# Kernel optimization log

Hardware: AMD Instinct MI355X
Metric: run time of the kernel (lower is better)

Reference implementation:

```python
import jax, jax.numpy as jnp
import numpy as np

N_NODES = 50000
N_EDGES = 800000
IN_CH = 1024
OUT_CH = 256


def setup_inputs() -> dict:
    key = jax.random.key(0)
    ks = jax.random.split(key, 7)
    x = jax.random.normal(ks[0], (N_NODES, IN_CH), dtype=jnp.float32)
    src_index = jax.random.randint(ks[1], (N_EDGES,), 0, N_NODES, dtype=jnp.int32)
    tar_index = jax.random.randint(ks[2], (N_EDGES,), 0, N_NODES, dtype=jnp.int32)
    edge_weight = jax.random.uniform(ks[3], (N_EDGES,), dtype=jnp.float32)
    self_edge_weight = jax.random.uniform(ks[4], (N_NODES,), dtype=jnp.float32)
    # Linear layer params (torch.nn.Linear: y = x @ W.T + b)
    bound = 1.0 / np.sqrt(IN_CH)
    W = jax.random.uniform(ks[5], (OUT_CH, IN_CH), dtype=jnp.float32, minval=-bound, maxval=bound)
    b = jax.random.uniform(ks[6], (OUT_CH,), dtype=jnp.float32, minval=-bound, maxval=bound)
    return {"x": x, "W": W, "b": b, "src_index": src_index, "tar_index": tar_index,
            "edge_weight": edge_weight, "self_edge_weight": self_edge_weight}


def reference(x, W, b, src_index, tar_index, edge_weight, self_edge_weight):
    # dense linear projection: [N, in] -> [N, out]
    h = jnp.einsum('ni,oi->no', x, W) + b
    # edge aggregation: out[t] += w_e * h[src_e]  (SpMM-like gather/scatter)
    msgs = h[src_index] * edge_weight[:, None]          # [E, out]
    agg = jax.ops.segment_sum(msgs, tar_index, num_segments=h.shape[0])
    # self-loop term
    return agg + self_edge_weight[:, None] * h
```

## Files before the change

### kernel.cpp

```cpp
#include <hip/hip_runtime.h>
#include <hip/hip_bf16.h>

#define N_NODES 50000
#define N_EDGES 800000
#define IN_CH 1024
#define OUT_CH 256
#define NBLK 196

typedef __attribute__((ext_vector_type(8))) short bf16x8;
typedef __attribute__((ext_vector_type(4))) float f32x4;

__device__ inline unsigned short f2bf(float f) {
  union { float f; unsigned int u; } v; v.f = f;
  unsigned int r = v.u + 0x7fffu + ((v.u >> 16) & 1u);
  return (unsigned short)(r >> 16);
}
__device__ inline float bf2f(unsigned short u) {
  union { unsigned int u; float f; } v; v.u = ((unsigned int)u) << 16;
  return v.f;
}

__global__ __launch_bounds__(256) void prep_hist(const float* __restrict__ W,
                                                 unsigned short* __restrict__ Wb,
                                                 const int* __restrict__ tar,
                                                 int* __restrict__ counts) {
  const int b = blockIdx.x, t = threadIdx.x;
  if (b < 256) {
    const int i4 = (b * 256 + t) * 4;
    float4 f = *(const float4*)(W + i4);
    *(ushort4*)(Wb + i4) = make_ushort4(f2bf(f.x), f2bf(f.y), f2bf(f.z), f2bf(f.w));
  } else {
    const int e = (b - 256) * 256 + t;
    if (e < N_EDGES) atomicAdd(&counts[tar[e]], 1);
  }
}

__global__ __launch_bounds__(256, 4) void gemm_proj(
    const float* __restrict__ X, const unsigned short* __restrict__ Wb,
    const float* __restrict__ bias, unsigned short* __restrict__ Hb)
{
  __shared__ unsigned short lds_a[2][64][32];
  __shared__ unsigned short lds_b[2][128][32];

  const int tid  = threadIdx.x;
  const int lane = tid & 63;
  const int w    = tid >> 6;
  const int wr   = w >> 1, wc = w & 1;
  const int gm0  = blockIdx.x * 64;
  const int gn0  = blockIdx.y * 128;

  const int ar = tid >> 3;
  const int ac = (tid & 7) * 4;
  const int br = tid >> 2;
  const int bc = (tid & 3) * 8;

  const int arow0 = gm0 + ar, arow1 = gm0 + ar + 32;
  const bool aok0 = arow0 < N_NODES, aok1 = arow1 < N_NODES;
  const float* xp0 = X + (size_t)arow0 * IN_CH + ac;
  const float* xp1 = X + (size_t)arow1 * IN_CH + ac;
  const unsigned short* wp0 = Wb + (size_t)(gn0 + br) * IN_CH + bc;
  const unsigned short* wp1 = Wb + (size_t)(gn0 + br + 64) * IN_CH + bc;

  f32x4 acc[2][4];
  #pragma unroll
  for (int i = 0; i < 2; i++)
    #pragma unroll
    for (int j = 0; j < 4; j++) acc[i][j] = (f32x4)0.0f;

  float4 avA0, avA1, avB0, avB1;
  bf16x8 bvA0, bvA1, bvB0, bvB1;

#define LOADR(KS, AV0, AV1, BV0, BV1)                                          \
  {                                                                            \
    const int k0_ = (KS) * 32;                                                 \
    AV0 = aok0 ? *(const float4*)(xp0 + k0_) : make_float4(0.f, 0.f, 0.f, 0.f);\
    AV1 = aok1 ? *(const float4*)(xp1 + k0_) : make_float4(0.f, 0.f, 0.f, 0.f);\
    BV0 = *(const bf16x8*)(wp0 + k0_);                                         \
    BV1 = *(const bf16x8*)(wp1 + k0_);                                         \
  }

#define WRITER(BUF, AV0, AV1, BV0, BV1)                                        \
  {                                                                            \
    *(ushort4*)&lds_a[BUF][ar][ac] =                                           \
        make_ushort4(f2bf(AV0.x), f2bf(AV0.y), f2bf(AV0.z), f2bf(AV0.w));      \
    *(ushort4*)&lds_a[BUF][ar + 32][ac] =                                      \
        make_ushort4(f2bf(AV1.x), f2bf(AV1.y), f2bf(AV1.z), f2bf(AV1.w));      \
    *(bf16x8*)&lds_b[BUF][br][bc]      = BV0;                                  \
    *(bf16x8*)&lds_b[BUF][br + 64][bc] = BV1;                                  \
  }

#define COMPUTE(BUF)                                                           \
  {                                                                            \
    const int l15_ = lane & 15;                                                \
    const int kb_  = (lane >> 4) * 8;                                          \
    bf16x8 a0 = *(const bf16x8*)&lds_a[BUF][wr * 32 + l15_][kb_];              \
    bf16x8 a1 = *(const bf16x8*)&lds_a[BUF][wr * 32 + 16 + l15_][kb_];         \
    bf16x8 b0 = *(const bf16x8*)&lds_b[BUF][wc * 64 + l15_][kb_];              \
    bf16x8 b1 = *(const bf16x8*)&lds_b[BUF][wc * 64 + 16 + l15_][kb_];         \
    bf16x8 b2 = *(const bf16x8*)&lds_b[BUF][wc * 64 + 32 + l15_][kb_];         \
    bf16x8 b3 = *(const bf16x8*)&lds_b[BUF][wc * 64 + 48 + l15_][kb_];         \
    acc[0][0] = __builtin_amdgcn_mfma_f32_16x16x32_bf16(a0, b0, acc[0][0], 0, 0, 0); \
    acc[0][1] = __builtin_amdgcn_mfma_f32_16x16x32_bf16(a0, b1, acc[0][1], 0, 0, 0); \
    acc[0][2] = __builtin_amdgcn_mfma_f32_16x16x32_bf16(a0, b2, acc[0][2], 0, 0, 0); \
    acc[0][3] = __builtin_amdgcn_mfma_f32_16x16x32_bf16(a0, b3, acc[0][3], 0, 0, 0); \
    acc[1][0] = __builtin_amdgcn_mfma_f32_16x16x32_bf16(a1, b0, acc[1][0], 0, 0, 0); \
    acc[1][1] = __builtin_amdgcn_mfma_f32_16x16x32_bf16(a1, b1, acc[1][1], 0, 0, 0); \
    acc[1][2] = __builtin_amdgcn_mfma_f32_16x16x32_bf16(a1, b2, acc[1][2], 0, 0, 0); \
    acc[1][3] = __builtin_amdgcn_mfma_f32_16x16x32_bf16(a1, b3, acc[1][3], 0, 0, 0); \
  }

  LOADR(0, avA0, avA1, bvA0, bvA1);
  WRITER(0, avA0, avA1, bvA0, bvA1);
  LOADR(1, avB0, avB1, bvB0, bvB1);
  __syncthreads();

  for (int ks = 0; ks < 32; ks += 2) {
    if (ks + 2 < 32) LOADR(ks + 2, avA0, avA1, bvA0, bvA1);
    COMPUTE(0);
    WRITER(1, avB0, avB1, bvB0, bvB1);
    __syncthreads();
    if (ks + 3 < 32) LOADR(ks + 3, avB0, avB1, bvB0, bvB1);
    COMPUTE(1);
    if (ks + 2 < 32) WRITER(0, avA0, avA1, bvA0, bvA1);
    __syncthreads();
  }
#undef LOADR
#undef WRITER
#undef COMPUTE

  float bj[4];
  #pragma unroll
  for (int j = 0; j < 4; j++)
    bj[j] = bias[gn0 + wc * 64 + j * 16 + (lane & 15)];

  #pragma unroll
  for (int i = 0; i < 2; i++) {
    const int grow_base = gm0 + wr * 32 + i * 16 + ((lane >> 4) << 2);
    #pragma unroll
    for (int r = 0; r < 4; r++) {
      const int grow = grow_base + r;
      if (grow < N_NODES) {
        #pragma unroll
        for (int j = 0; j < 4; j++) {
          const int gcol = gn0 + wc * 64 + j * 16 + (lane & 15);
          Hb[(size_t)grow * OUT_CH + gcol] = f2bf(acc[i][j][r] + bj[j]);
        }
      }
    }
  }
}

__global__ __launch_bounds__(256) void scan_block(const int* __restrict__ counts,
                                                  int* __restrict__ offsets,
                                                  int* __restrict__ blocksum) {
  __shared__ int wsum[4];
  const int tid = threadIdx.x, lane = tid & 63, wv = tid >> 6;
  const int i = blockIdx.x * 256 + tid;
  const int v = (i < N_NODES) ? counts[i] : 0;
  int s = v;
  #pragma unroll
  for (int off = 1; off < 64; off <<= 1) {
    int t = __shfl_up(s, off, 64);
    if (lane >= off) s += t;
  }
  if (lane == 63) wsum[wv] = s;
  __syncthreads();
  if (tid == 0) {
    int c = 0;
    #pragma unroll
    for (int k = 0; k < 4; k++) { int t = wsum[k]; wsum[k] = c; c += t; }
  }
  __syncthreads();
  const int excl = wsum[wv] + s - v;
  if (i < N_NODES) offsets[i] = excl;
  if (tid == 255) blocksum[blockIdx.x] = excl + v;
}

__global__ __launch_bounds__(256) void scan_sums(int* __restrict__ blocksum,
                                                 int* __restrict__ offsets) {
  __shared__ int wsum[4];
  const int tid = threadIdx.x, lane = tid & 63, wv = tid >> 6;
  const int v = (tid < NBLK) ? blocksum[tid] : 0;
  int s = v;
  #pragma unroll
  for (int off = 1; off < 64; off <<= 1) {
    int t = __shfl_up(s, off, 64);
    if (lane >= off) s += t;
  }
  if (lane == 63) wsum[wv] = s;
  __syncthreads();
  if (tid == 0) {
    int c = 0;
    #pragma unroll
    for (int k = 0; k < 4; k++) { int t = wsum[k]; wsum[k] = c; c += t; }
  }
  __syncthreads();
  const int excl = wsum[wv] + s - v;
  if (tid < NBLK) blocksum[tid] = excl;
  if (tid == 255) offsets[N_NODES] = excl;
}

__global__ __launch_bounds__(256) void finalize_offsets(int* __restrict__ offsets,
                                                        const int* __restrict__ blocksum,
                                                        int* __restrict__ cursor) {
  const int i = blockIdx.x * 256 + threadIdx.x;
  if (i < N_NODES) {
    const int off = offsets[i] + blocksum[i >> 8];
    offsets[i] = off;
    cursor[i] = off;
  }
}

__global__ __launch_bounds__(256) void fill_csr(const int* __restrict__ src,
                                                const int* __restrict__ tar,
                                                const float* __restrict__ ew,
                                                int* __restrict__ cursor,
                                                int2* __restrict__ edata) {
  int e = blockIdx.x * blockDim.x + threadIdx.x;
  if (e >= N_EDGES) return;
  const int t = tar[e];
  const int p = atomicAdd(&cursor[t], 1);
  edata[p] = make_int2(src[e], __float_as_int(ew[e]));
}

__global__ __launch_bounds__(256) void node_agg(
    const unsigned short* __restrict__ Hb, const int* __restrict__ offsets,
    const int2* __restrict__ edata, const float* __restrict__ sw,
    float* __restrict__ OUT)
{
  const int wid = (blockIdx.x * blockDim.x + threadIdx.x) >> 6;
  if (wid >= N_NODES) return;
  const int lane = threadIdx.x & 63;
  const int e0 = offsets[wid];
  const int e1 = offsets[wid + 1];

  float a0 = 0.f, a1 = 0.f, a2 = 0.f, a3 = 0.f;

  for (int base = e0; base < e1; base += 64) {
    const int avail = e1 - base;
    int2 d = make_int2(0, 0);
    if (lane < avail) d = edata[base + lane];
    const int n = (avail < 64) ? avail : 64;
    int j = 0;
    for (; j + 4 <= n; j += 4) {
      const int   s0 = __shfl(d.x, j, 64),     s1 = __shfl(d.x, j + 1, 64);
      const int   s2 = __shfl(d.x, j + 2, 64), s3 = __shfl(d.x, j + 3, 64);
      const float w0 = __int_as_float(__shfl(d.y, j, 64));
      const float w1 = __int_as_float(__shfl(d.y, j + 1, 64));
      const float w2 = __int_as_float(__shfl(d.y, j + 2, 64));
      const float w3 = __int_as_float(__shfl(d.y, j + 3, 64));
      const ushort4 h0 = *(const ushort4*)(Hb + (size_t)s0 * OUT_CH + lane * 4);
      const ushort4 h1 = *(const ushort4*)(Hb + (size_t)s1 * OUT_CH + lane * 4);
      const ushort4 h2 = *(const ushort4*)(Hb + (size_t)s2 * OUT_CH + lane * 4);
      const ushort4 h3 = *(const ushort4*)(Hb + (size_t)s3 * OUT_CH + lane * 4);
      a0 += w0 * bf2f(h0.x) + w1 * bf2f(h1.x) + w2 * bf2f(h2.x) + w3 * bf2f(h3.x);
      a1 += w0 * bf2f(h0.y) + w1 * bf2f(h1.y) + w2 * bf2f(h2.y) + w3 * bf2f(h3.y);
      a2 += w0 * bf2f(h0.z) + w1 * bf2f(h1.z) + w2 * bf2f(h2.z) + w3 * bf2f(h3.z);
      a3 += w0 * bf2f(h0.w) + w1 * bf2f(h1.w) + w2 * bf2f(h2.w) + w3 * bf2f(h3.w);
    }
    for (; j < n; j++) {
      const int   s = __shfl(d.x, j, 64);
      const float wgt = __int_as_float(__shfl(d.y, j, 64));
      const ushort4 h = *(const ushort4*)(Hb + (size_t)s * OUT_CH + lane * 4);
      a0 += wgt * bf2f(h.x); a1 += wgt * bf2f(h.y);
      a2 += wgt * bf2f(h.z); a3 += wgt * bf2f(h.w);
    }
  }

  const float swv = sw[wid];
  const ushort4 hs = *(const ushort4*)(Hb + (size_t)wid * OUT_CH + lane * 4);
  float4 o;
  o.x = a0 + swv * bf2f(hs.x);
  o.y = a1 + swv * bf2f(hs.y);
  o.z = a2 + swv * bf2f(hs.z);
  o.w = a3 + swv * bf2f(hs.w);
  *(float4*)(OUT + (size_t)wid * OUT_CH + lane * 4) = o;
}

extern "C" void kernel_launch(void* const* d_in, const int* in_sizes, int n_in,
                              void* d_out, int out_size, void* d_ws, size_t ws_size,
                              hipStream_t stream) {
  const float* x   = (const float*)d_in[0];
  const float* W   = (const float*)d_in[1];
  const float* b   = (const float*)d_in[2];
  const int*   src = (const int*)d_in[3];
  const int*   tar = (const int*)d_in[4];
  const float* ew  = (const float*)d_in[5];
  const float* sw  = (const float*)d_in[6];
  float* out = (float*)d_out;

  char* ws = (char*)d_ws;
  size_t o = 0;
  unsigned short* Wb = (unsigned short*)(ws + o);
  o += (size_t)OUT_CH * IN_CH * 2;          o = (o + 255) & ~(size_t)255;
  unsigned short* Hb = (unsigned short*)(ws + o);
  o += (size_t)N_NODES * OUT_CH * 2;        o = (o + 255) & ~(size_t)255;
  int* counts   = (int*)(ws + o); o += (size_t)N_NODES * 4;       o = (o + 255) & ~(size_t)255;
  int* offsets  = (int*)(ws + o); o += (size_t)(N_NODES + 1) * 4; o = (o + 255) & ~(size_t)255;
  int* cursor   = (int*)(ws + o); o += (size_t)N_NODES * 4;       o = (o + 255) & ~(size_t)255;
  int* blocksum = (int*)(ws + o); o += (size_t)NBLK * 4;          o = (o + 255) & ~(size_t)255;
  int2* edata   = (int2*)(ws + o);

  hipMemsetAsync(counts, 0, (size_t)N_NODES * 4, stream);
  prep_hist<<<256 + (N_EDGES + 255) / 256, 256, 0, stream>>>(W, Wb, tar, counts);
  scan_block<<<NBLK, 256, 0, stream>>>(counts, offsets, blocksum);
  scan_sums<<<1, 256, 0, stream>>>(blocksum, offsets);
  finalize_offsets<<<NBLK, 256, 0, stream>>>(offsets, blocksum, cursor);
  fill_csr<<<(N_EDGES + 255) / 256, 256, 0, stream>>>(src, tar, ew, cursor, edata);

  dim3 g1((N_NODES + 63) / 64, OUT_CH / 128);
  gemm_proj<<<g1, 256, 0, stream>>>(x, Wb, b, Hb);

  const long long nthreads = (long long)N_NODES * 64;
  node_agg<<<(int)((nthreads + 255) / 256), 256, 0, stream>>>(Hb, offsets, edata, sw, out);
}
```

Before: 244.0 us.

## Deepen X prefetch pipeline to three stages and use packed bf16 conversion

The GEMM projection now prefetches X tiles three k-steps ahead in a 3-slot register ring, while W stays two steps ahead. The loop is fully unrolled with one barrier per step. The f32-to-bf16 conversion of X uses the hardware v_cvt_pk_bf16_f32 instruction instead of the manual rounding sequence. More registers are needed, so launch bounds drop from 4 to 3 blocks per CU, trading occupancy for deeper latency hiding of the X loads.

```diff
diff --git a/kernel.cpp b/kernel.cpp
--- a/kernel.cpp
+++ b/kernel.cpp
@@ -18,6 +18,11 @@
 __device__ inline float bf2f(unsigned short u) {
   union { unsigned int u; float f; } v; v.u = ((unsigned int)u) << 16;
   return v.f;
+}
+__device__ inline unsigned int cvtpk_bf16(float a, float b) {
+  unsigned int r;
+  asm("v_cvt_pk_bf16_f32 %0, %1, %2" : "=v"(r) : "v"(a), "v"(b));
+  return r;
 }
 
 __global__ __launch_bounds__(256) void prep_hist(const float* __restrict__ W,
@@ -35,7 +40,7 @@
   }
 }
 
-__global__ __launch_bounds__(256, 4) void gemm_proj(
+__global__ __launch_bounds__(256, 3) void gemm_proj(
     const float* __restrict__ X, const unsigned short* __restrict__ Wb,
     const float* __restrict__ bias, unsigned short* __restrict__ Hb)
 {
@@ -67,28 +72,34 @@
     #pragma unroll
     for (int j = 0; j < 4; j++) acc[i][j] = (f32x4)0.0f;
 
-  float4 avA0, avA1, avB0, avB1;
-  bf16x8 bvA0, bvA1, bvB0, bvB1;
-
-#define LOADR(KS, AV0, AV1, BV0, BV1)                                          \
+  float4 pa[3][2];
+  bf16x8 pb[2][2];
+
+#define LOADA(KS, SL)                                                          \
   {                                                                            \
     const int k0_ = (KS) * 32;                                                 \
-    AV0 = aok0 ? *(const float4*)(xp0 + k0_) : make_float4(0.f, 0.f, 0.f, 0.f);\
-    AV1 = aok1 ? *(const float4*)(xp1 + k0_) : make_float4(0.f, 0.f, 0.f, 0.f);\
-    BV0 = *(const bf16x8*)(wp0 + k0_);                                         \
-    BV1 = *(const bf16x8*)(wp1 + k0_);                                         \
-  }
-
-#define WRITER(BUF, AV0, AV1, BV0, BV1)                                        \
+    pa[SL][0] = aok0 ? *(const float4*)(xp0 + k0_)                             \
+                     : make_float4(0.f, 0.f, 0.f, 0.f);                        \
+    pa[SL][1] = aok1 ? *(const float4*)(xp1 + k0_)                             \
+                     : make_float4(0.f, 0.f, 0.f, 0.f);                        \
+  }
+#define LOADB(KS, SL)                                                          \
   {                                                                            \
-    *(ushort4*)&lds_a[BUF][ar][ac] =                                           \
-        make_ushort4(f2bf(AV0.x), f2bf(AV0.y), f2bf(AV0.z), f2bf(AV0.w));      \
-    *(ushort4*)&lds_a[BUF][ar + 32][ac] =                                      \
-        make_ushort4(f2bf(AV1.x), f2bf(AV1.y), f2bf(AV1.z), f2bf(AV1.w));      \
-    *(bf16x8*)&lds_b[BUF][br][bc]      = BV0;                                  \
-    *(bf16x8*)&lds_b[BUF][br + 64][bc] = BV1;                                  \
-  }
-
+    const int k0_ = (KS) * 32;                                                 \
+    pb[SL][0] = *(const bf16x8*)(wp0 + k0_);                                   \
+    pb[SL][1] = *(const bf16x8*)(wp1 + k0_);                                   \
+  }
+#define WRITER(BUF, SA, SB)                                                    \
+  {                                                                            \
+    *(uint2*)&lds_a[BUF][ar][ac] =                                             \
+        make_uint2(cvtpk_bf16(pa[SA][0].x, pa[SA][0].y),                       \
+                   cvtpk_bf16(pa[SA][0].z, pa[SA][0].w));                      \
+    *(uint2*)&lds_a[BUF][ar + 32][ac] =                                        \
+        make_uint2(cvtpk_bf16(pa[SA][1].x, pa[SA][1].y),                       \
+                   cvtpk_bf16(pa[SA][1].z, pa[SA][1].w));                      \
+    *(bf16x8*)&lds_b[BUF][br][bc]      = pb[SB][0];                            \
+    *(bf16x8*)&lds_b[BUF][br + 64][bc] = pb[SB][1];                            \
+  }
 #define COMPUTE(BUF)                                                           \
   {                                                                            \
     const int l15_ = lane & 15;                                                \
@@ -109,22 +120,21 @@
     acc[1][3] = __builtin_amdgcn_mfma_f32_16x16x32_bf16(a1, b3, acc[1][3], 0, 0, 0); \
   }
 
-  LOADR(0, avA0, avA1, bvA0, bvA1);
-  WRITER(0, avA0, avA1, bvA0, bvA1);
-  LOADR(1, avB0, avB1, bvB0, bvB1);
-  __syncthreads();
-
-  for (int ks = 0; ks < 32; ks += 2) {
-    if (ks + 2 < 32) LOADR(ks + 2, avA0, avA1, bvA0, bvA1);
-    COMPUTE(0);
-    WRITER(1, avB0, avB1, bvB0, bvB1);
+  LOADA(0, 0); LOADA(1, 1); LOADA(2, 2);
+  LOADB(0, 0); LOADB(1, 1);
+  WRITER(0, 0, 0);
+  __syncthreads();
+
+  #pragma unroll
+  for (int ks = 0; ks < 32; ks++) {
+    if (ks + 3 < 32) LOADA(ks + 3, (ks + 3) % 3);
+    if (ks + 2 < 32) LOADB(ks + 2, ks & 1);
+    COMPUTE(ks & 1);
+    if (ks + 1 < 32) WRITER((ks + 1) & 1, (ks + 1) % 3, (ks + 1) & 1);
     __syncthreads();
-    if (ks + 3 < 32) LOADR(ks + 3, avB0, avB1, bvB0, bvB1);
-    COMPUTE(1);
-    if (ks + 2 < 32) WRITER(0, avA0, avA1, bvA0, bvA1);
-    __syncthreads();
-  }
-#undef LOADR
+  }
+#undef LOADA
+#undef LOADB
 #undef WRITER
 #undef COMPUTE
 
```

Measured after the change: 236.3 us. 3.2% less time.

## Deepen GEMM K-tile to 64 with swizzled LDS and unroll gather by 8

Applied to the files above, without the earlier changes.

The projection GEMM now stages 64-wide K slices per step instead of 32, halving the number of barrier-separated iterations. Its LDS layout gains an XOR swizzle to avoid bank conflicts, and the float-to-bf16 conversion uses the packed v_cvt_pk_bf16_f32 instruction. The edge-gather loop now issues eight row loads before accumulating, up from four, to increase memory-level parallelism. The costs are more LDS and registers per block, which the launch bound lowers from 4 to 3 blocks per CU, reducing occupancy.

```diff
diff --git a/kernel.cpp b/kernel.cpp
--- a/kernel.cpp
+++ b/kernel.cpp
@@ -18,6 +18,11 @@
 __device__ inline float bf2f(unsigned short u) {
   union { unsigned int u; float f; } v; v.u = ((unsigned int)u) << 16;
   return v.f;
+}
+__device__ inline unsigned int cvtpk_bf16(float a, float b) {
+  unsigned int r;
+  asm("v_cvt_pk_bf16_f32 %0, %1, %2" : "=v"(r) : "v"(a), "v"(b));
+  return r;
 }
 
 __global__ __launch_bounds__(256) void prep_hist(const float* __restrict__ W,
@@ -35,12 +40,12 @@
   }
 }
 
-__global__ __launch_bounds__(256, 4) void gemm_proj(
+__global__ __launch_bounds__(256, 3) void gemm_proj(
     const float* __restrict__ X, const unsigned short* __restrict__ Wb,
     const float* __restrict__ bias, unsigned short* __restrict__ Hb)
 {
-  __shared__ unsigned short lds_a[2][64][32];
-  __shared__ unsigned short lds_b[2][128][32];
+  __shared__ unsigned short lds_a[2][64][64];
+  __shared__ unsigned short lds_b[2][128][64];
 
   const int tid  = threadIdx.x;
   const int lane = tid & 63;
@@ -48,18 +53,19 @@
   const int wr   = w >> 1, wc = w & 1;
   const int gm0  = blockIdx.x * 64;
   const int gn0  = blockIdx.y * 128;
-
-  const int ar = tid >> 3;
-  const int ac = (tid & 7) * 4;
-  const int br = tid >> 2;
-  const int bc = (tid & 3) * 8;
-
-  const int arow0 = gm0 + ar, arow1 = gm0 + ar + 32;
-  const bool aok0 = arow0 < N_NODES, aok1 = arow1 < N_NODES;
-  const float* xp0 = X + (size_t)arow0 * IN_CH + ac;
-  const float* xp1 = X + (size_t)arow1 * IN_CH + ac;
-  const unsigned short* wp0 = Wb + (size_t)(gn0 + br) * IN_CH + bc;
-  const unsigned short* wp1 = Wb + (size_t)(gn0 + br + 64) * IN_CH + bc;
+  const int l15  = lane & 15;
+  const int hi   = lane >> 4;
+
+  const int ar  = tid >> 2;
+  const int ac0 = (tid & 3) * 2;
+  const int br  = tid >> 1;
+  const int bc0 = (tid & 1) * 4;
+
+  const int  arow = gm0 + ar;
+  const bool aok  = arow < N_NODES;
+  const float* xp = X + (size_t)arow * IN_CH;
+  const unsigned short* wp = Wb + (size_t)(gn0 + br) * IN_CH;
+  const float4 fz = make_float4(0.f, 0.f, 0.f, 0.f);
 
   f32x4 acc[2][4];
   #pragma unroll
@@ -67,61 +73,81 @@
     #pragma unroll
     for (int j = 0; j < 4; j++) acc[i][j] = (f32x4)0.0f;
 
-  float4 avA0, avA1, avB0, avB1;
-  bf16x8 bvA0, bvA1, bvB0, bvB1;
-
-#define LOADR(KS, AV0, AV1, BV0, BV1)                                          \
+  float4 pa[2][4];
+  bf16x8 pbv[2][4];
+
+#define LOADR(KS, S)                                                           \
   {                                                                            \
-    const int k0_ = (KS) * 32;                                                 \
-    AV0 = aok0 ? *(const float4*)(xp0 + k0_) : make_float4(0.f, 0.f, 0.f, 0.f);\
-    AV1 = aok1 ? *(const float4*)(xp1 + k0_) : make_float4(0.f, 0.f, 0.f, 0.f);\
-    BV0 = *(const bf16x8*)(wp0 + k0_);                                         \
-    BV1 = *(const bf16x8*)(wp1 + k0_);                                         \
-  }
-
-#define WRITER(BUF, AV0, AV1, BV0, BV1)                                        \
+    const int k0_ = (KS) * 64;                                                 \
+    const float* xa_ = xp + k0_ + ac0 * 8;                                     \
+    pa[S][0] = aok ? *(const float4*)(xa_)      : fz;                          \
+    pa[S][1] = aok ? *(const float4*)(xa_ + 4)  : fz;                          \
+    pa[S][2] = aok ? *(const float4*)(xa_ + 8)  : fz;                          \
+    pa[S][3] = aok ? *(const float4*)(xa_ + 12) : fz;                          \
+    const unsigned short* wb_ = wp + k0_ + bc0 * 8;                            \
+    pbv[S][0] = *(const bf16x8*)(wb_);                                         \
+    pbv[S][1] = *(const bf16x8*)(wb_ + 8);                                     \
+    pbv[S][2] = *(const bf16x8*)(wb_ + 16);                                    \
+    pbv[S][3] = *(const bf16x8*)(wb_ + 24);                                    \
+  }
+
+#define WRITER(BUF, S)                                                         \
   {                                                                            \
-    *(ushort4*)&lds_a[BUF][ar][ac] =                                           \
-        make_ushort4(f2bf(AV0.x), f2bf(AV0.y), f2bf(AV0.z), f2bf(AV0.w));      \
-    *(ushort4*)&lds_a[BUF][ar + 32][ac] =                                      \
-        make_ushort4(f2bf(AV1.x), f2bf(AV1.y), f2bf(AV1.z), f2bf(AV1.w));      \
-    *(bf16x8*)&lds_b[BUF][br][bc]      = BV0;                                  \
-    *(bf16x8*)&lds_b[BUF][br + 64][bc] = BV1;                                  \
+    const int pc0_ = ac0 ^ (ar & 7);                                           \
+    const int pc1_ = (ac0 + 1) ^ (ar & 7);                                     \
+    union { unsigned int u[4]; bf16x8 v; } ta_;                                \
+    ta_.u[0] = cvtpk_bf16(pa[S][0].x, pa[S][0].y);                             \
+    ta_.u[1] = cvtpk_bf16(pa[S][0].z, pa[S][0].w);                             \
+    ta_.u[2] = cvtpk_bf16(pa[S][1].x, pa[S][1].y);                             \
+    ta_.u[3] = cvtpk_bf16(pa[S][1].z, pa[S][1].w);                             \
+    *(bf16x8*)&lds_a[BUF][ar][pc0_ * 8] = ta_.v;                               \
+    ta_.u[0] = cvtpk_bf16(pa[S][2].x, pa[S][2].y);                             \
+    ta_.u[1] = cvtpk_bf16(pa[S][2].z, pa[S][2].w);                             \
+    ta_.u[2] = cvtpk_bf16(pa[S][3].x, pa[S][3].y);                             \
+    ta_.u[3] = cvtpk_bf16(pa[S][3].z, pa[S][3].w);                             \
+    *(bf16x8*)&lds_a[BUF][ar][pc1_ * 8] = ta_.v;                               \
+    _Pragma("unroll")                                                          \
+    for (int q = 0; q < 4; q++) {                                              \
+      const int pcb_ = (bc0 + q) ^ (br & 7);                                   \
+      *(bf16x8*)&lds_b[BUF][br][pcb_ * 8] = pbv[S][q];                         \
+    }                                                                          \
   }
 
 #define COMPUTE(BUF)                                                           \
   {                                                                            \
-    const int l15_ = lane & 15;                                                \
-    const int kb_  = (lane >> 4) * 8;                                          \
-    bf16x8 a0 = *(const bf16x8*)&lds_a[BUF][wr * 32 + l15_][kb_];              \
-    bf16x8 a1 = *(const bf16x8*)&lds_a[BUF][wr * 32 + 16 + l15_][kb_];         \
-    bf16x8 b0 = *(const bf16x8*)&lds_b[BUF][wc * 64 + l15_][kb_];              \
-    bf16x8 b1 = *(const bf16x8*)&lds_b[BUF][wc * 64 + 16 + l15_][kb_];         \
-    bf16x8 b2 = *(const bf16x8*)&lds_b[BUF][wc * 64 + 32 + l15_][kb_];         \
-    bf16x8 b3 = *(const bf16x8*)&lds_b[BUF][wc * 64 + 48 + l15_][kb_];         \
-    acc[0][0] = __builtin_amdgcn_mfma_f32_16x16x32_bf16(a0, b0, acc[0][0], 0, 0, 0); \
-    acc[0][1] = __builtin_amdgcn_mfma_f32_16x16x32_bf16(a0, b1, acc[0][1], 0, 0, 0); \
-    acc[0][2] = __builtin_amdgcn_mfma_f32_16x16x32_bf16(a0, b2, acc[0][2], 0, 0, 0); \
-    acc[0][3] = __builtin_amdgcn_mfma_f32_16x16x32_bf16(a0, b3, acc[0][3], 0, 0, 0); \
-    acc[1][0] = __builtin_amdgcn_mfma_f32_16x16x32_bf16(a1, b0, acc[1][0], 0, 0, 0); \
-    acc[1][1] = __builtin_amdgcn_mfma_f32_16x16x32_bf16(a1, b1, acc[1][1], 0, 0, 0); \
-    acc[1][2] = __builtin_amdgcn_mfma_f32_16x16x32_bf16(a1, b2, acc[1][2], 0, 0, 0); \
-    acc[1][3] = __builtin_amdgcn_mfma_f32_16x16x32_bf16(a1, b3, acc[1][3], 0, 0, 0); \
-  }
-
-  LOADR(0, avA0, avA1, bvA0, bvA1);
-  WRITER(0, avA0, avA1, bvA0, bvA1);
-  LOADR(1, avB0, avB1, bvB0, bvB1);
-  __syncthreads();
-
-  for (int ks = 0; ks < 32; ks += 2) {
-    if (ks + 2 < 32) LOADR(ks + 2, avA0, avA1, bvA0, bvA1);
+    _Pragma("unroll")                                                          \
+    for (int kk2 = 0; kk2 < 2; kk2++) {                                        \
+      const int pc_ = ((kk2 << 2) + hi) ^ (l15 & 7);                           \
+      bf16x8 a0 = *(const bf16x8*)&lds_a[BUF][wr * 32 + l15][pc_ * 8];         \
+      bf16x8 a1 = *(const bf16x8*)&lds_a[BUF][wr * 32 + 16 + l15][pc_ * 8];    \
+      bf16x8 b0 = *(const bf16x8*)&lds_b[BUF][wc * 64 + l15][pc_ * 8];         \
+      bf16x8 b1 = *(const bf16x8*)&lds_b[BUF][wc * 64 + 16 + l15][pc_ * 8];    \
+      bf16x8 b2 = *(const bf16x8*)&lds_b[BUF][wc * 64 + 32 + l15][pc_ * 8];    \
+      bf16x8 b3 = *(const bf16x8*)&lds_b[BUF][wc * 64 + 48 + l15][pc_ * 8];    \
+      acc[0][0] = __builtin_amdgcn_mfma_f32_16x16x32_bf16(a0, b0, acc[0][0], 0, 0, 0); \
+      acc[0][1] = __builtin_amdgcn_mfma_f32_16x16x32_bf16(a0, b1, acc[0][1], 0, 0, 0); \
+      acc[0][2] = __builtin_amdgcn_mfma_f32_16x16x32_bf16(a0, b2, acc[0][2], 0, 0, 0); \
+      acc[0][3] = __builtin_amdgcn_mfma_f32_16x16x32_bf16(a0, b3, acc[0][3], 0, 0, 0); \
+      acc[1][0] = __builtin_amdgcn_mfma_f32_16x16x32_bf16(a1, b0, acc[1][0], 0, 0, 0); \
+      acc[1][1] = __builtin_amdgcn_mfma_f32_16x16x32_bf16(a1, b1, acc[1][1], 0, 0, 0); \
+      acc[1][2] = __builtin_amdgcn_mfma_f32_16x16x32_bf16(a1, b2, acc[1][2], 0, 0, 0); \
+      acc[1][3] = __builtin_amdgcn_mfma_f32_16x16x32_bf16(a1, b3, acc[1][3], 0, 0, 0); \
+    }                                                                          \
+  }
+
+  LOADR(0, 0);
+  WRITER(0, 0);
+  LOADR(1, 1);
+  __syncthreads();
+
+  for (int ks = 0; ks < 16; ks += 2) {
+    if (ks + 2 < 16) LOADR(ks + 2, 0);
     COMPUTE(0);
-    WRITER(1, avB0, avB1, bvB0, bvB1);
+    WRITER(1, 1);
     __syncthreads();
-    if (ks + 3 < 32) LOADR(ks + 3, avB0, avB1, bvB0, bvB1);
+    if (ks + 3 < 16) LOADR(ks + 3, 1);
     COMPUTE(1);
-    if (ks + 2 < 32) WRITER(0, avA0, avA1, bvA0, bvA1);
+    if (ks + 2 < 16) WRITER(0, 0);
     __syncthreads();
   }
 #undef LOADR
@@ -131,18 +157,18 @@
   float bj[4];
   #pragma unroll
   for (int j = 0; j < 4; j++)
-    bj[j] = bias[gn0 + wc * 64 + j * 16 + (lane & 15)];
+    bj[j] = bias[gn0 + wc * 64 + j * 16 + l15];
 
   #pragma unroll
   for (int i = 0; i < 2; i++) {
-    const int grow_base = gm0 + wr * 32 + i * 16 + ((lane >> 4) << 2);
+    const int grow_base = gm0 + wr * 32 + i * 16 + hi * 4;
     #pragma unroll
     for (int r = 0; r < 4; r++) {
       const int grow = grow_base + r;
       if (grow < N_NODES) {
         #pragma unroll
         for (int j = 0; j < 4; j++) {
-          const int gcol = gn0 + wc * 64 + j * 16 + (lane & 15);
+          const int gcol = gn0 + wc * 64 + j * 16 + l15;
           Hb[(size_t)grow * OUT_CH + gcol] = f2bf(acc[i][j][r] + bj[j]);
         }
       }
@@ -242,21 +268,25 @@
     if (lane < avail) d = edata[base + lane];
     const int n = (avail < 64) ? avail : 64;
     int j = 0;
-    for (; j + 4 <= n; j += 4) {
-      const int   s0 = __shfl(d.x, j, 64),     s1 = __shfl(d.x, j + 1, 64);
-      const int   s2 = __shfl(d.x, j + 2, 64), s3 = __shfl(d.x, j + 3, 64);
-      const float w0 = __int_as_float(__shfl(d.y, j, 64));
-      const float w1 = __int_as_float(__shfl(d.y, j + 1, 64));
-      const float w2 = __int_as_float(__shfl(d.y, j + 2, 64));
-      const float w3 = __int_as_float(__shfl(d.y, j + 3, 64));
-      const ushort4 h0 = *(const ushort4*)(Hb + (size_t)s0 * OUT_CH + lane * 4);
-      const ushort4 h1 = *(const ushort4*)(Hb + (size_t)s1 * OUT_CH + lane * 4);
-      const ushort4 h2 = *(const ushort4*)(Hb + (size_t)s2 * OUT_CH + lane * 4);
-      const ushort4 h3 = *(const ushort4*)(Hb + (size_t)s3 * OUT_CH + lane * 4);
-      a0 += w0 * bf2f(h0.x) + w1 * bf2f(h1.x) + w2 * bf2f(h2.x) + w3 * bf2f(h3.x);
-      a1 += w0 * bf2f(h0.y) + w1 * bf2f(h1.y) + w2 * bf2f(h2.y) + w3 * bf2f(h3.y);
-      a2 += w0 * bf2f(h0.z) + w1 * bf2f(h1.z) + w2 * bf2f(h2.z) + w3 * bf2f(h3.z);
-      a3 += w0 * bf2f(h0.w) + w1 * bf2f(h1.w) + w2 * bf2f(h2.w) + w3 * bf2f(h3.w);
+    for (; j + 8 <= n; j += 8) {
+      int   sE[8];
+      float wE[8];
+      #pragma unroll
+      for (int q = 0; q < 8; q++) {
+        sE[q] = __shfl(d.x, j + q, 64);
+        wE[q] = __int_as_float(__shfl(d.y, j + q, 64));
+      }
+      ushort4 hE[8];
+      #pragma unroll
+      for (int q = 0; q < 8; q++)
+        hE[q] = *(const ushort4*)(Hb + (size_t)sE[q] * OUT_CH + lane * 4);
+      #pragma unroll
+      for (int q = 0; q < 8; q++) {
+        a0 += wE[q] * bf2f(hE[q].x);
+        a1 += wE[q] * bf2f(hE[q].y);
+        a2 += wE[q] * bf2f(hE[q].z);
+        a3 += wE[q] * bf2f(hE[q].w);
+      }
     }
     for (; j < n; j++) {
       const int   s = __shfl(d.x, j, 64);
```

New measurement: 397.6 us. 1.63x slower.
